# Performance work log

Measured on AMD Instinct MI355X. Metric: run time of the kernel, lower is better.

The kernel has to match this reference:

```python
import jax, jax.numpy as jnp
import numpy as np

B, S, D, H, E, K, F = 2, 2048, 1024, 16, 8, 2, 4096
DH = D // H
EPS = 1e-5


def setup_inputs() -> dict:
    key = jax.random.key(0)
    ks = jax.random.split(key, 10)
    init = lambda k, shape, scale: (jax.random.normal(k, shape, jnp.float32) * scale)
    s_d = D ** -0.5
    s_f = F ** -0.5
    return {
        "x": init(ks[0], (B, S, D), 1.0),
        "attn_mask": jnp.tril(jnp.ones((S, S), bool)),  # causal boolean mask
        "wq": init(ks[1], (D, D), s_d),
        "wk": init(ks[2], (D, D), s_d),
        "wv": init(ks[3], (D, D), s_d),
        "wo": init(ks[4], (D, D), s_d),
        "ln1_g": jnp.ones((D,), jnp.float32),
        "ln1_b": jnp.zeros((D,), jnp.float32),
        "ln2_g": jnp.ones((D,), jnp.float32),
        "ln2_b": jnp.zeros((D,), jnp.float32),
        "gate_w": init(ks[5], (D, E), s_d),
        "e_w1": init(ks[6], (E, D, F), s_d),
        "e_b1": jnp.zeros((E, F), jnp.float32),
        "e_w2": init(ks[7], (E, F, D), s_f),
        "e_b2": jnp.zeros((E, D), jnp.float32),
    }


def _ln(x, g, b):
    m = x.mean(-1, keepdims=True)
    v = ((x - m) ** 2).mean(-1, keepdims=True)
    return (x - m) * jax.lax.rsqrt(v + EPS) * g + b


def _mha(x, attn_mask, wq, wk, wv, wo):
    # x: [B,S,D] -> q,k,v: [B,H,S,DH]
    q = (x @ wq).reshape(B, S, H, DH).transpose(0, 2, 1, 3)
    k = (x @ wk).reshape(B, S, H, DH).transpose(0, 2, 1, 3)
    v = (x @ wv).reshape(B, S, H, DH).transpose(0, 2, 1, 3)
    scores = jnp.einsum("bhqd,bhkd->bhqk", q, k) * (DH ** -0.5)
    scores = jnp.where(attn_mask, scores, jnp.finfo(scores.dtype).min)
    attn = jax.nn.softmax(scores, axis=-1)
    o = jnp.einsum("bhqk,bhkd->bhqd", attn, v)
    return o.transpose(0, 2, 1, 3).reshape(B, S, D) @ wo


def _moe(x, gate_w, e_w1, e_b1, e_w2, e_b2):
    tokens = x.reshape(-1, D)  # [N,D]
    logits = tokens @ gate_w   # [N,E]
    vals, idx = jax.lax.top_k(logits, K)
    tw = jax.nn.softmax(vals, axis=-1)  # softmax over selected top-k logits
    # dense per-token expert weight matrix [N,E] (zero for unselected experts)
    w_dense = (jax.nn.one_hot(idx, E, dtype=tokens.dtype) * tw[..., None]).sum(1)

    def step(acc, p):
        w1, b1, w2, b2, we = p
        h = jax.nn.gelu(tokens @ w1 + b1)
        return acc + (h @ w2 + b2) * we[:, None], None

    combined, _ = jax.lax.scan(
        step, jnp.zeros_like(tokens), (e_w1, e_b1, e_w2, e_b2, w_dense.T)
    )
    return combined.reshape(x.shape)


def reference(x, attn_mask, wq, wk, wv, wo, ln1_g, ln1_b, ln2_g, ln2_b,
              gate_w, e_w1, e_b1, e_w2, e_b2):
    x = _ln(x, ln1_g, ln1_b)
    x = x + _mha(x, attn_mask, wq, wk, wv, wo)  # dropout p=0.0
    x = _ln(x, ln2_g, ln2_b)
    x = x + _moe(x, gate_w, e_w1, e_b1, e_w2, e_b2)
    return x
```

## Files before the change

### kernel.cpp

```cpp
#include <hip/hip_runtime.h>
#include <math.h>
#include <stdint.h>

typedef __attribute__((ext_vector_type(8))) short short8;
typedef __attribute__((ext_vector_type(4))) float f32x4;
typedef __attribute__((ext_vector_type(4))) unsigned short u16x4;

#define NB 2
#define NS 2048
#define ND 1024
#define NH 16
#define NDH 64
#define NE 8
#define NF 4096
#define NTOK 4096
#define MAXBLK 72

__device__ __forceinline__ float bf2f(unsigned short u) {
  union { float f; uint32_t i; } x; x.i = ((uint32_t)u) << 16; return x.f;
}
__device__ __forceinline__ unsigned short f2bf(float f) {
  union { float f; uint32_t i; } x; x.f = f;
  uint32_t r = x.i + 0x7fffu + ((x.i >> 16) & 1u);
  return (unsigned short)(r >> 16);
}
struct bfp { unsigned short h, l; };
__device__ __forceinline__ bfp splitf(float x) {
  bfp r;
  r.h = f2bf(x);
  r.l = f2bf(x - bf2f(r.h));
  return r;
}
__device__ __forceinline__ float gelu_f(float x) {
  float u = 0.7978845608028654f * (x + 0.044715f * x * x * x);
  return 0.5f * x * (1.0f + tanhf(u));
}
#define MFMA(a, b, c) __builtin_amdgcn_mfma_f32_16x16x32_bf16(a, b, c, 0, 0, 0)
__device__ __forceinline__ f32x4 mfma4(short8 ah, short8 al, short8 bh, short8 bl,
                                       f32x4 c) {
  c = MFMA(ah, bh, c);
  c = MFMA(ah, bl, c);
  c = MFMA(al, bh, c);
  c = MFMA(al, bl, c);
  return c;
}

__global__ __launch_bounds__(256) void ln_kernel(
    const float* __restrict__ x, const float* __restrict__ g,
    const float* __restrict__ b, unsigned short* __restrict__ out_h,
    unsigned short* __restrict__ out_l, unsigned short* __restrict__ out_b16,
    float* __restrict__ out_f) {
  int row = blockIdx.x;
  int tid = threadIdx.x;
  const float* xr = x + (size_t)row * ND;
  f32x4 v = *(const f32x4*)(xr + tid * 4);
  float s = v[0] + v[1] + v[2] + v[3];
  float s2 = v[0]*v[0] + v[1]*v[1] + v[2]*v[2] + v[3]*v[3];
  for (int o = 1; o < 64; o <<= 1) { s += __shfl_xor(s, o); s2 += __shfl_xor(s2, o); }
  __shared__ float red[8];
  if ((tid & 63) == 0) { red[tid >> 6] = s; red[4 + (tid >> 6)] = s2; }
  __syncthreads();
  s = red[0] + red[1] + red[2] + red[3];
  s2 = red[4] + red[5] + red[6] + red[7];
  float mean = s * (1.0f / ND);
  float var = s2 * (1.0f / ND) - mean * mean;
  float rstd = rsqrtf(var + 1e-5f);
  f32x4 gg = *(const f32x4*)(g + tid * 4);
  f32x4 bb = *(const f32x4*)(b + tid * 4);
  f32x4 of;
#pragma unroll
  for (int j = 0; j < 4; j++) of[j] = (v[j] - mean) * rstd * gg[j] + bb[j];
  *(f32x4*)(out_f + (size_t)row * ND + tid * 4) = of;
  if (out_h) {
    u16x4 oh, ol;
#pragma unroll
    for (int j = 0; j < 4; j++) { bfp t = splitf(of[j]); oh[j] = t.h; ol[j] = t.l; }
    *(u16x4*)(out_h + (size_t)row * ND + tid * 4) = oh;
    *(u16x4*)(out_l + (size_t)row * ND + tid * 4) = ol;
  }
  if (out_b16) {
    u16x4 ob;
#pragma unroll
    for (int j = 0; j < 4; j++) ob[j] = f2bf(of[j]);
    *(u16x4*)(out_b16 + (size_t)row * ND + tid * 4) = ob;
  }
}

__global__ __launch_bounds__(256) void transpose_wsplit(
    const float* __restrict__ in, unsigned short* __restrict__ outh,
    unsigned short* __restrict__ outl, int R, int C) {
  __shared__ float tile[64][68];
  int r0 = blockIdx.y * 64, c0 = blockIdx.x * 64;
  int lr = threadIdx.x >> 3, lc = (threadIdx.x & 7) * 8;
#pragma unroll
  for (int p = 0; p < 2; p++) {
    int r = lr + p * 32;
    const float* s = in + (size_t)(r0 + r) * C + c0 + lc;
    *(f32x4*)&tile[r][lc] = *(const f32x4*)s;
    *(f32x4*)&tile[r][lc + 4] = *(const f32x4*)(s + 4);
  }
  __syncthreads();
#pragma unroll
  for (int p = 0; p < 2; p++) {
    int c = lr + p * 32;
    u16x4 h0, h1, l0, l1;
#pragma unroll
    for (int i = 0; i < 4; i++) {
      bfp t0 = splitf(tile[lc + i][c]);
      bfp t1 = splitf(tile[lc + 4 + i][c]);
      h0[i] = t0.h; l0[i] = t0.l;
      h1[i] = t1.h; l1[i] = t1.l;
    }
    unsigned short* dh = outh + (size_t)(c0 + c) * R + r0 + lc;
    unsigned short* dl = outl + (size_t)(c0 + c) * R + r0 + lc;
    *(u16x4*)dh = h0; *(u16x4*)(dh + 4) = h1;
    *(u16x4*)dl = l0; *(u16x4*)(dl + 4) = l1;
  }
}

__global__ __launch_bounds__(256) void transpose_w(
    const float* __restrict__ in, unsigned short* __restrict__ out,
    int R, int C) {
  __shared__ unsigned short tile[64][72];
  const float* src = in + (size_t)blockIdx.z * R * C;
  unsigned short* dst = out + (size_t)blockIdx.z * R * C;
  int r0 = blockIdx.y * 64, c0 = blockIdx.x * 64;
  int lr = threadIdx.x >> 3, lc = (threadIdx.x & 7) * 8;
#pragma unroll
  for (int p = 0; p < 2; p++) {
    int r = lr + p * 32;
    const float* s = src + (size_t)(r0 + r) * C + c0 + lc;
    f32x4 a = *(const f32x4*)s;
    f32x4 b = *(const f32x4*)(s + 4);
    u16x4 t0, t1;
#pragma unroll
    for (int j = 0; j < 4; j++) { t0[j] = f2bf(a[j]); t1[j] = f2bf(b[j]); }
    *(u16x4*)&tile[r][lc] = t0;
    *(u16x4*)&tile[r][lc + 4] = t1;
  }
  __syncthreads();
#pragma unroll
  for (int p = 0; p < 2; p++) {
    int c = lr + p * 32;
    union { unsigned short s[8]; f32x4 v; } t;
#pragma unroll
    for (int i = 0; i < 8; i++) t.s[i] = tile[lc + i][c];
    *(f32x4*)(dst + (size_t)(c0 + c) * R + r0 + lc) = t.v;
  }
}

__global__ __launch_bounds__(256) void transpose_v_split(
    const float* __restrict__ v_lin, unsigned short* __restrict__ vth,
    unsigned short* __restrict__ vtl) {
  __shared__ float tile[64][68];
  int bh = blockIdx.y, b = bh >> 4, h = bh & 15;
  int s0 = blockIdx.x * 64;
  int lr = threadIdx.x >> 3, lc = (threadIdx.x & 7) * 8;
#pragma unroll
  for (int p = 0; p < 2; p++) {
    int s = lr + p * 32;
    const float* src = v_lin + (size_t)(b * NS + s0 + s) * ND + h * NDH + lc;
    *(f32x4*)&tile[s][lc] = *(const f32x4*)src;
    *(f32x4*)&tile[s][lc + 4] = *(const f32x4*)(src + 4);
  }
  __syncthreads();
#pragma unroll
  for (int p = 0; p < 2; p++) {
    int dh = lr + p * 32;
    u16x4 h0, h1, l0, l1;
#pragma unroll
    for (int i = 0; i < 4; i++) {
      bfp t0 = splitf(tile[lc + i][dh]);
      bfp t1 = splitf(tile[lc + 4 + i][dh]);
      h0[i] = t0.h; l0[i] = t0.l;
      h1[i] = t1.h; l1[i] = t1.l;
    }
    unsigned short* dh_p = vth + (size_t)(bh * NDH + dh) * NS + s0 + lc;
    unsigned short* dl_p = vtl + (size_t)(bh * NDH + dh) * NS + s0 + lc;
    *(u16x4*)dh_p = h0; *(u16x4*)(dh_p + 4) = h1;
    *(u16x4*)dl_p = l0; *(u16x4*)(dl_p + 4) = l1;
  }
}

template <int MODE>
__global__ __launch_bounds__(256, 2) void gemm_bsplit(
    const unsigned short* __restrict__ Ah, const unsigned short* __restrict__ Al,
    const unsigned short* __restrict__ Bh, const unsigned short* __restrict__ Bl,
    const float* __restrict__ res, float* __restrict__ Cf,
    unsigned short* __restrict__ Ch, unsigned short* __restrict__ Cl,
    int N, int K) {
  __shared__ unsigned short sAh[128 * 72];
  __shared__ unsigned short sAl[128 * 72];
  __shared__ unsigned short sBh[128 * 72];
  __shared__ unsigned short sBl[128 * 72];
  int m0 = blockIdx.y * 128, n0 = blockIdx.x * 128;
  int tid = threadIdx.x;
  int lane = tid & 63, wid = tid >> 6;
  int wy = wid >> 1, wx = wid & 1;
  int col = lane & 15, quad = lane >> 4;
  int srow = tid >> 3, scol = (tid & 7) * 8;
  const unsigned short* ah_p[4];
  const unsigned short* al_p[4];
  const unsigned short* bh_p[4];
  const unsigned short* bl_p[4];
#pragma unroll
  for (int g = 0; g < 4; g++) {
    size_t ao = (size_t)(m0 + g * 32 + srow) * K + scol;
    size_t bo = (size_t)(n0 + g * 32 + srow) * K + scol;
    ah_p[g] = Ah + ao; al_p[g] = Al + ao;
    bh_p[g] = Bh + bo; bl_p[g] = Bl + bo;
  }
  f32x4 acc[4][4];
#pragma unroll
  for (int mt = 0; mt < 4; mt++)
#pragma unroll
    for (int nt = 0; nt < 4; nt++) acc[mt][nt] = (f32x4){0.f, 0.f, 0.f, 0.f};

  for (int k0 = 0; k0 < K; k0 += 64) {
    f32x4 rah[4], ral[4], rbh[4], rbl[4];
#pragma unroll
    for (int g = 0; g < 4; g++) {
      rah[g] = *(const f32x4*)(ah_p[g] + k0);
      ral[g] = *(const f32x4*)(al_p[g] + k0);
      rbh[g] = *(const f32x4*)(bh_p[g] + k0);
      rbl[g] = *(const f32x4*)(bl_p[g] + k0);
    }
    __syncthreads();
#pragma unroll
    for (int g = 0; g < 4; g++) {
      int ro = (g * 32 + srow) * 72 + scol;
      *(f32x4*)(sAh + ro) = rah[g];
      *(f32x4*)(sAl + ro) = ral[g];
      *(f32x4*)(sBh + ro) = rbh[g];
      *(f32x4*)(sBl + ro) = rbl[g];
    }
    __syncthreads();
#pragma unroll
    for (int kk = 0; kk < 2; kk++) {
      short8 ah[4], al[4], bh[4], bl[4];
#pragma unroll
      for (int mt = 0; mt < 4; mt++) {
        int o = (wy * 64 + mt * 16 + col) * 72 + kk * 32 + quad * 8;
        ah[mt] = *(const short8*)(sAh + o);
        al[mt] = *(const short8*)(sAl + o);
      }
#pragma unroll
      for (int nt = 0; nt < 4; nt++) {
        int o = (wx * 64 + nt * 16 + col) * 72 + kk * 32 + quad * 8;
        bh[nt] = *(const short8*)(sBh + o);
        bl[nt] = *(const short8*)(sBl + o);
      }
#pragma unroll
      for (int mt = 0; mt < 4; mt++)
#pragma unroll
        for (int nt = 0; nt < 4; nt++)
          acc[mt][nt] = mfma4(ah[mt], al[mt], bh[nt], bl[nt], acc[mt][nt]);
    }
  }
#pragma unroll
  for (int mt = 0; mt < 4; mt++)
#pragma unroll
    for (int nt = 0; nt < 4; nt++)
#pragma unroll
      for (int r = 0; r < 4; r++) {
        int gr = m0 + wy * 64 + mt * 16 + quad * 4 + r;
        int gc = n0 + wx * 64 + nt * 16 + col;
        float v = acc[mt][nt][r];
        if (MODE == 1) v += res[(size_t)gr * N + gc];
        if (MODE == 2) {
          bfp t = splitf(v);
          Ch[(size_t)gr * N + gc] = t.h;
          Cl[(size_t)gr * N + gc] = t.l;
        } else {
          Cf[(size_t)gr * N + gc] = v;
        }
      }
}

__global__ __launch_bounds__(256, 2) void attn_kernel(
    const unsigned short* __restrict__ qh_g, const unsigned short* __restrict__ ql_g,
    const unsigned short* __restrict__ kh_g, const unsigned short* __restrict__ kl_g,
    const unsigned short* __restrict__ vth_g, const unsigned short* __restrict__ vtl_g,
    unsigned short* __restrict__ oh_g, unsigned short* __restrict__ ol_g) {
  __shared__ unsigned short Kh[64 * 72];
  __shared__ unsigned short Kl[64 * 72];
  __shared__ unsigned short Vh[64 * 72];
  __shared__ unsigned short Vl[64 * 72];
  __shared__ unsigned short Ph[64 * 72];
  __shared__ unsigned short Pl[64 * 72];
  int bh = blockIdx.y, b = bh >> 4, h = bh & 15;
  int tid = threadIdx.x, lane = tid & 63, w = tid >> 6;
  int col = lane & 15, quad = lane >> 4;
  int lr = tid >> 3, lc = (tid & 7) * 8;

  const unsigned short* kbh = kh_g + (size_t)b * NS * ND + h * NDH + lc;
  const unsigned short* kbl = kl_g + (size_t)b * NS * ND + h * NDH + lc;
  const unsigned short* vbh = vth_g + (size_t)bh * NDH * NS;
  const unsigned short* vbl = vtl_g + (size_t)bh * NDH * NS;

#pragma unroll 1
  for (int pass = 0; pass < 2; pass++) {
    int qt = (pass == 0) ? (int)blockIdx.x : 31 - (int)blockIdx.x;
    int q0 = qt * 64;

    size_t qoff = (size_t)(b * NS + q0 + w * 16 + col) * ND + h * NDH;
    short8 qh0 = *(const short8*)(qh_g + qoff + quad * 8);
    short8 qh1 = *(const short8*)(qh_g + qoff + 32 + quad * 8);
    short8 ql0 = *(const short8*)(ql_g + qoff + quad * 8);
    short8 ql1 = *(const short8*)(ql_g + qoff + 32 + quad * 8);

    f32x4 Oa[4];
#pragma unroll
    for (int nt = 0; nt < 4; nt++) Oa[nt] = (f32x4){0.f, 0.f, 0.f, 0.f};
    float mrow[4] = {-1e30f, -1e30f, -1e30f, -1e30f};
    float lrow[4] = {0.f, 0.f, 0.f, 0.f};

    for (int j = 0; j <= qt; j++) {
      __syncthreads();
#pragma unroll
      for (int p = 0; p < 2; p++) {
        int r = lr + p * 32;
        size_t ko = (size_t)(j * 64 + r) * ND;
        size_t vo = (size_t)r * NS + j * 64 + lc;
        *(f32x4*)(Kh + r * 72 + lc) = *(const f32x4*)(kbh + ko);
        *(f32x4*)(Kl + r * 72 + lc) = *(const f32x4*)(kbl + ko);
        *(f32x4*)(Vh + r * 72 + lc) = *(const f32x4*)(vbh + vo);
        *(f32x4*)(Vl + r * 72 + lc) = *(const f32x4*)(vbl + vo);
      }
      __syncthreads();
      f32x4 sf[4];
      __builtin_amdgcn_s_setprio(1);
#pragma unroll
      for (int nt = 0; nt < 4; nt++) {
        int o0 = (nt * 16 + col) * 72 + quad * 8;
        f32x4 a = (f32x4){0.f, 0.f, 0.f, 0.f};
        a = mfma4(qh0, ql0, *(const short8*)(Kh + o0), *(const short8*)(Kl + o0), a);
        a = mfma4(qh1, ql1, *(const short8*)(Kh + o0 + 32), *(const short8*)(Kl + o0 + 32), a);
        sf[nt] = a;
      }
      __builtin_amdgcn_s_setprio(0);
      bool diag = (j == qt);
#pragma unroll
      for (int nt = 0; nt < 4; nt++)
#pragma unroll
        for (int r = 0; r < 4; r++) {
          float v = sf[nt][r] * 0.125f;
          if (diag) {
            int rq = w * 16 + quad * 4 + r;
            int ck = nt * 16 + col;
            if (ck > rq) v = -1e30f;
          }
          sf[nt][r] = v;
        }
#pragma unroll
      for (int r = 0; r < 4; r++) {
        float mx = fmaxf(fmaxf(sf[0][r], sf[1][r]), fmaxf(sf[2][r], sf[3][r]));
        mx = fmaxf(mx, __shfl_xor(mx, 1));
        mx = fmaxf(mx, __shfl_xor(mx, 2));
        mx = fmaxf(mx, __shfl_xor(mx, 4));
        mx = fmaxf(mx, __shfl_xor(mx, 8));
        float mn = fmaxf(mrow[r], mx);
        float al = __expf(mrow[r] - mn);
        mrow[r] = mn;
        float ps = 0.f;
#pragma unroll
        for (int nt = 0; nt < 4; nt++) {
          float p = __expf(sf[nt][r] - mn);
          sf[nt][r] = p;
          ps += p;
        }
        ps += __shfl_xor(ps, 1);
        ps += __shfl_xor(ps, 2);
        ps += __shfl_xor(ps, 4);
        ps += __shfl_xor(ps, 8);
        lrow[r] = lrow[r] * al + ps;
#pragma unroll
        for (int nt = 0; nt < 4; nt++) Oa[nt][r] *= al;
      }
#pragma unroll
      for (int nt = 0; nt < 4; nt++)
#pragma unroll
        for (int r = 0; r < 4; r++) {
          bfp t = splitf(sf[nt][r]);
          int o = (w * 16 + quad * 4 + r) * 72 + nt * 16 + col;
          Ph[o] = t.h;
          Pl[o] = t.l;
        }
      __syncthreads();
      int po = (w * 16 + col) * 72 + quad * 8;
      short8 pf0h = *(const short8*)(Ph + po);
      short8 pf0l = *(const short8*)(Pl + po);
      short8 pf1h = *(const short8*)(Ph + po + 32);
      short8 pf1l = *(const short8*)(Pl + po + 32);
      __builtin_amdgcn_s_setprio(1);
#pragma unroll
      for (int nt = 0; nt < 4; nt++) {
        int o0 = (nt * 16 + col) * 72 + quad * 8;
        Oa[nt] = mfma4(pf0h, pf0l, *(const short8*)(Vh + o0), *(const short8*)(Vl + o0), Oa[nt]);
        Oa[nt] = mfma4(pf1h, pf1l, *(const short8*)(Vh + o0 + 32), *(const short8*)(Vl + o0 + 32), Oa[nt]);
      }
      __builtin_amdgcn_s_setprio(0);
    }
#pragma unroll
    for (int nt = 0; nt < 4; nt++)
#pragma unroll
      for (int r = 0; r < 4; r++) {
        int gr = q0 + w * 16 + quad * 4 + r;
        int gc = nt * 16 + col;
        float ov = Oa[nt][r] / lrow[r];
        bfp t = splitf(ov);
        size_t oo = (size_t)(b * NS + gr) * ND + h * NDH + gc;
        oh_g[oo] = t.h;
        ol_g[oo] = t.l;
      }
  }
}

__device__ __forceinline__ void gemm_mainloop(
    const unsigned short* ap0, const unsigned short* ap1,
    const unsigned short* ap2, const unsigned short* ap3,
    const unsigned short* bp0, const unsigned short* bp1,
    const unsigned short* bp2, const unsigned short* bp3, int K,
    unsigned short* As, unsigned short* Bs, f32x4 acc[4][4]) {
  const int tid = threadIdx.x;
  const int lane = tid & 63, wid = tid >> 6;
  const int wy = wid >> 1, wx = wid & 1;
  const int col = lane & 15, quad = lane >> 4;
  const int srow = tid >> 3, scol = (tid & 7) * 8;
  for (int k0 = 0; k0 < K; k0 += 64) {
    f32x4 ra0 = *(const f32x4*)(ap0 + k0);
    f32x4 ra1 = *(const f32x4*)(ap1 + k0);
    f32x4 ra2 = *(const f32x4*)(ap2 + k0);
    f32x4 ra3 = *(const f32x4*)(ap3 + k0);
    f32x4 rb0 = *(const f32x4*)(bp0 + k0);
    f32x4 rb1 = *(const f32x4*)(bp1 + k0);
    f32x4 rb2 = *(const f32x4*)(bp2 + k0);
    f32x4 rb3 = *(const f32x4*)(bp3 + k0);
    __syncthreads();
    *(f32x4*)(As + (size_t)(srow) * 72 + scol) = ra0;
    *(f32x4*)(As + (size_t)(srow + 32) * 72 + scol) = ra1;
    *(f32x4*)(As + (size_t)(srow + 64) * 72 + scol) = ra2;
    *(f32x4*)(As + (size_t)(srow + 96) * 72 + scol) = ra3;
    *(f32x4*)(Bs + (size_t)(srow) * 72 + scol) = rb0;
    *(f32x4*)(Bs + (size_t)(srow + 32) * 72 + scol) = rb1;
    *(f32x4*)(Bs + (size_t)(srow + 64) * 72 + scol) = rb2;
    *(f32x4*)(Bs + (size_t)(srow + 96) * 72 + scol) = rb3;
    __syncthreads();
#pragma unroll
    for (int kk = 0; kk < 2; kk++) {
      short8 af[4], bfv[4];
#pragma unroll
      for (int mt = 0; mt < 4; mt++)
        af[mt] = *(const short8*)(As + (wy * 64 + mt * 16 + col) * 72 + kk * 32 + quad * 8);
#pragma unroll
      for (int nt = 0; nt < 4; nt++)
        bfv[nt] = *(const short8*)(Bs + (wx * 64 + nt * 16 + col) * 72 + kk * 32 + quad * 8);
#pragma unroll
      for (int mt = 0; mt < 4; mt++)
#pragma unroll
        for (int nt = 0; nt < 4; nt++)
          acc[mt][nt] = MFMA(af[mt], bfv[nt], acc[mt][nt]);
    }
  }
}

__global__ __launch_bounds__(256, 2) void gemm_moe1(
    const unsigned short* __restrict__ x3b, const unsigned short* __restrict__ w1t,
    const float* __restrict__ b1, const int* __restrict__ blk_e,
    const int* __restrict__ blk_mend, const int* __restrict__ tok_list,
    unsigned short* __restrict__ h) {
  __shared__ unsigned short As[128 * 72];
  __shared__ unsigned short Bs[128 * 72];
  int e = blk_e[blockIdx.y];
  if (e < 0) return;
  int mend = blk_mend[blockIdx.y];
  int m0 = blockIdx.y * 128, n0 = blockIdx.x * 128;
  int tid = threadIdx.x;
  int srow = tid >> 3, scol = (tid & 7) * 8;
  const unsigned short* ap[4];
#pragma unroll
  for (int p = 0; p < 4; p++) {
    int gidx = m0 + p * 32 + srow;
    int cl = mend - 1;
    if (gidx < cl) cl = gidx;
    int tok = tok_list[cl];
    ap[p] = x3b + (size_t)tok * ND + scol;
  }
  const unsigned short* bb = w1t + (size_t)e * NF * ND;
  const unsigned short* bp0 = bb + (size_t)(n0 + srow) * ND + scol;
  const unsigned short* bp1 = bb + (size_t)(n0 + 32 + srow) * ND + scol;
  const unsigned short* bp2 = bb + (size_t)(n0 + 64 + srow) * ND + scol;
  const unsigned short* bp3 = bb + (size_t)(n0 + 96 + srow) * ND + scol;
  f32x4 acc[4][4];
#pragma unroll
  for (int mt = 0; mt < 4; mt++)
#pragma unroll
    for (int nt = 0; nt < 4; nt++) acc[mt][nt] = (f32x4){0.f, 0.f, 0.f, 0.f};
  gemm_mainloop(ap[0], ap[1], ap[2], ap[3], bp0, bp1, bp2, bp3, ND, As, Bs, acc);
  int lane = tid & 63, wid = tid >> 6, wy = wid >> 1, wx = wid & 1;
  int col = lane & 15, quad = lane >> 4;
#pragma unroll
  for (int mt = 0; mt < 4; mt++)
#pragma unroll
    for (int nt = 0; nt < 4; nt++)
#pragma unroll
      for (int r = 0; r < 4; r++) {
        int gr = m0 + wy * 64 + mt * 16 + quad * 4 + r;
        if (gr < mend) {
          int gc = n0 + wx * 64 + nt * 16 + col;
          float v = acc[mt][nt][r] + b1[e * NF + gc];
          h[(size_t)gr * NF + gc] = f2bf(gelu_f(v));
        }
      }
}

__global__ __launch_bounds__(256, 2) void gemm_moe2(
    const unsigned short* __restrict__ h, const unsigned short* __restrict__ w2t,
    const float* __restrict__ b2, const int* __restrict__ blk_e,
    const int* __restrict__ blk_mend, const int* __restrict__ tok_list,
    const float* __restrict__ w_list, float* __restrict__ out) {
  __shared__ unsigned short As[128 * 72];
  __shared__ unsigned short Bs[128 * 72];
  int e = blk_e[blockIdx.y];
  if (e < 0) return;
  int mend = blk_mend[blockIdx.y];
  int m0 = blockIdx.y * 128, n0 = blockIdx.x * 128;
  int tid = threadIdx.x;
  int srow = tid >> 3, scol = (tid & 7) * 8;
  const unsigned short* ap0 = h + (size_t)(m0 + srow) * NF + scol;
  const unsigned short* ap1 = h + (size_t)(m0 + 32 + srow) * NF + scol;
  const unsigned short* ap2 = h + (size_t)(m0 + 64 + srow) * NF + scol;
  const unsigned short* ap3 = h + (size_t)(m0 + 96 + srow) * NF + scol;
  const unsigned short* bb = w2t + (size_t)e * ND * NF;
  const unsigned short* bp0 = bb + (size_t)(n0 + srow) * NF + scol;
  const unsigned short* bp1 = bb + (size_t)(n0 + 32 + srow) * NF + scol;
  const unsigned short* bp2 = bb + (size_t)(n0 + 64 + srow) * NF + scol;
  const unsigned short* bp3 = bb + (size_t)(n0 + 96 + srow) * NF + scol;
  f32x4 acc[4][4];
#pragma unroll
  for (int mt = 0; mt < 4; mt++)
#pragma unroll
    for (int nt = 0; nt < 4; nt++) acc[mt][nt] = (f32x4){0.f, 0.f, 0.f, 0.f};
  gemm_mainloop(ap0, ap1, ap2, ap3, bp0, bp1, bp2, bp3, NF, As, Bs, acc);
  int lane = tid & 63, wid = tid >> 6, wy = wid >> 1, wx = wid & 1;
  int col = lane & 15, quad = lane >> 4;
#pragma unroll
  for (int mt = 0; mt < 4; mt++)
#pragma unroll
    for (int nt = 0; nt < 4; nt++)
#pragma unroll
      for (int r = 0; r < 4; r++) {
        int gr = m0 + wy * 64 + mt * 16 + quad * 4 + r;
        if (gr < mend) {
          int gc = n0 + wx * 64 + nt * 16 + col;
          int tok = tok_list[gr];
          float wgt = w_list[gr];
          atomicAdd(&out[(size_t)tok * ND + gc],
                    wgt * (acc[mt][nt][r] + b2[e * ND + gc]));
        }
      }
}

__global__ __launch_bounds__(256) void gate_kernel(
    const float* __restrict__ x3f, const float* __restrict__ gw,
    int* __restrict__ e0a, int* __restrict__ e1a, float* __restrict__ w0a,
    float* __restrict__ w1a, int* __restrict__ cnt) {
  int t = (blockIdx.x * 256 + threadIdx.x) >> 6;
  int lane = threadIdx.x & 63;
  float acc[8] = {0, 0, 0, 0, 0, 0, 0, 0};
  const float* xr = x3f + (size_t)t * ND + lane * 16;
  f32x4 xv[4];
#pragma unroll
  for (int q = 0; q < 4; q++) xv[q] = *(const f32x4*)(xr + q * 4);
#pragma unroll
  for (int i = 0; i < 16; i++) {
    float xval = xv[i >> 2][i & 3];
    const float* grow = gw + (size_t)(lane * 16 + i) * NE;
    f32x4 g0 = *(const f32x4*)grow;
    f32x4 g1 = *(const f32x4*)(grow + 4);
#pragma unroll
    for (int e = 0; e < 4; e++) { acc[e] += xval * g0[e]; acc[4 + e] += xval * g1[e]; }
  }
#pragma unroll
  for (int e = 0; e < 8; e++)
    for (int o = 1; o < 64; o <<= 1) acc[e] += __shfl_xor(acc[e], o);
  if (lane == 0) {
    int i0 = 0;
    float m0 = acc[0];
#pragma unroll
    for (int e = 1; e < 8; e++)
      if (acc[e] > m0) { m0 = acc[e]; i0 = e; }
    int i1 = -1;
    float m1 = -1e30f;
#pragma unroll
    for (int e = 0; e < 8; e++)
      if (e != i0 && acc[e] > m1) { m1 = acc[e]; i1 = e; }
    float sw = __expf(m1 - m0);
    float w0 = 1.f / (1.f + sw);
    e0a[t] = i0; e1a[t] = i1; w0a[t] = w0; w1a[t] = 1.f - w0;
    atomicAdd(&cnt[i0], 1);
    atomicAdd(&cnt[i1], 1);
  }
}

__global__ void moe_scan(const int* __restrict__ cnt, int* __restrict__ seg_off,
                         int* __restrict__ blk_e, int* __restrict__ blk_mend) {
  if (threadIdx.x != 0 || blockIdx.x != 0) return;
  int o = 0, blk = 0;
  for (int e = 0; e < NE; e++) {
    seg_off[e] = o;
    int c = cnt[e];
    int nb = (c + 127) >> 7;
    for (int i = 0; i < nb; i++) { blk_e[blk] = e; blk_mend[blk] = o + c; blk++; }
    o += nb << 7;
  }
  for (; blk < MAXBLK; blk++) blk_e[blk] = -1;
}

__global__ __launch_bounds__(256) void gate_fill(
    const int* __restrict__ e0a, const int* __restrict__ e1a,
    const float* __restrict__ w0a, const float* __restrict__ w1a,
    const int* __restrict__ seg_off, int* __restrict__ fill,
    int* __restrict__ tok_list, float* __restrict__ w_list) {
  int t = blockIdx.x * 256 + threadIdx.x;
  if (t >= NTOK) return;
  int e0 = e0a[t];
  int p0 = seg_off[e0] + atomicAdd(&fill[e0], 1);
  tok_list[p0] = t;
  w_list[p0] = w0a[t];
  int e1 = e1a[t];
  int p1 = seg_off[e1] + atomicAdd(&fill[e1], 1);
  tok_list[p1] = t;
  w_list[p1] = w1a[t];
}

extern "C" void kernel_launch(void* const* d_in, const int* in_sizes, int n_in,
                              void* d_out, int out_size, void* d_ws, size_t ws_size,
                              hipStream_t stream) {
  const float* x = (const float*)d_in[0];
  const float* wq = (const float*)d_in[2];
  const float* wk = (const float*)d_in[3];
  const float* wv = (const float*)d_in[4];
  const float* wo = (const float*)d_in[5];
  const float* ln1g = (const float*)d_in[6];
  const float* ln1b = (const float*)d_in[7];
  const float* ln2g = (const float*)d_in[8];
  const float* ln2b = (const float*)d_in[9];
  const float* gatew = (const float*)d_in[10];
  const float* ew1 = (const float*)d_in[11];
  const float* eb1 = (const float*)d_in[12];
  const float* ew2 = (const float*)d_in[13];
  const float* eb2 = (const float*)d_in[14];
  float* out = (float*)d_out;
  uint8_t* ws = (uint8_t*)d_ws;

  constexpr size_t MB = 1048576;
  constexpr size_t X1F = 0;
  constexpr size_t X1H = 16 * MB;
  constexpr size_t X1L = 24 * MB;
  constexpr size_t QH = 32 * MB;
  constexpr size_t QL = 40 * MB;
  constexpr size_t KH = 48 * MB;
  constexpr size_t KL = 56 * MB;
  constexpr size_t VF = 64 * MB;
  constexpr size_t OH = 64 * MB;
  constexpr size_t OL = 72 * MB;
  constexpr size_t VTH = 80 * MB;
  constexpr size_t VTL = 88 * MB;
  constexpr size_t X2F = 96 * MB;
  constexpr size_t WQTH = 112 * MB;
  constexpr size_t WQTL = 114 * MB;
  constexpr size_t WKTH = 116 * MB;
  constexpr size_t WKTL = 118 * MB;
  constexpr size_t WVTH = 120 * MB;
  constexpr size_t WVTL = 122 * MB;
  constexpr size_t WOTH = 124 * MB;
  constexpr size_t WOTL = 126 * MB;
  constexpr size_t X3B = 128 * MB;
  constexpr size_t HBUF = 136 * MB;
  constexpr size_t W1T = 0;
  constexpr size_t W2T = 64 * MB;
  constexpr size_t CTRL = 208 * MB;
  constexpr size_t CNT = CTRL;
  constexpr size_t FILL = CNT + 32;
  constexpr size_t GE0 = CNT + 64;
  constexpr size_t GE1 = GE0 + 16384;
  constexpr size_t GW0 = GE1 + 16384;
  constexpr size_t GW1 = GW0 + 16384;
  constexpr size_t SEGO = GW1 + 16384;
  constexpr size_t BLKE = SEGO + 64;
  constexpr size_t BLKM = BLKE + 512;
  constexpr size_t TOKL = BLKM + 512;
  constexpr size_t WLST = TOKL + 36864;

  float* pX1F = (float*)(ws + X1F);
  unsigned short* pX1H = (unsigned short*)(ws + X1H);
  unsigned short* pX1L = (unsigned short*)(ws + X1L);
  unsigned short* pQH = (unsigned short*)(ws + QH);
  unsigned short* pQL = (unsigned short*)(ws + QL);
  unsigned short* pKH = (unsigned short*)(ws + KH);
  unsigned short* pKL = (unsigned short*)(ws + KL);
  float* pVF = (float*)(ws + VF);
  unsigned short* pOH = (unsigned short*)(ws + OH);
  unsigned short* pOL = (unsigned short*)(ws + OL);
  unsigned short* pVTH = (unsigned short*)(ws + VTH);
  unsigned short* pVTL = (unsigned short*)(ws + VTL);
  float* pX2F = (float*)(ws + X2F);
  unsigned short* pWQTH = (unsigned short*)(ws + WQTH);
  unsigned short* pWQTL = (unsigned short*)(ws + WQTL);
  unsigned short* pWKTH = (unsigned short*)(ws + WKTH);
  unsigned short* pWKTL = (unsigned short*)(ws + WKTL);
  unsigned short* pWVTH = (unsigned short*)(ws + WVTH);
  unsigned short* pWVTL = (unsigned short*)(ws + WVTL);
  unsigned short* pWOTH = (unsigned short*)(ws + WOTH);
  unsigned short* pWOTL = (unsigned short*)(ws + WOTL);
  unsigned short* pX3B = (unsigned short*)(ws + X3B);
  unsigned short* pH = (unsigned short*)(ws + HBUF);
  unsigned short* pW1T = (unsigned short*)(ws + W1T);
  unsigned short* pW2T = (unsigned short*)(ws + W2T);
  int* pCNT = (int*)(ws + CNT);
  int* pFILL = (int*)(ws + FILL);
  int* pGE0 = (int*)(ws + GE0);
  int* pGE1 = (int*)(ws + GE1);
  float* pGW0 = (float*)(ws + GW0);
  float* pGW1 = (float*)(ws + GW1);
  int* pSEGO = (int*)(ws + SEGO);
  int* pBLKE = (int*)(ws + BLKE);
  int* pBLKM = (int*)(ws + BLKM);
  int* pTOKL = (int*)(ws + TOKL);
  float* pWLST = (float*)(ws + WLST);

  (void)hipMemsetAsync(ws + CNT, 0, 64, stream);

  ln_kernel<<<NTOK, 256, 0, stream>>>(x, ln1g, ln1b, pX1H, pX1L, nullptr, pX1F);

  transpose_wsplit<<<dim3(16, 16), 256, 0, stream>>>(wq, pWQTH, pWQTL, 1024, 1024);
  transpose_wsplit<<<dim3(16, 16), 256, 0, stream>>>(wk, pWKTH, pWKTL, 1024, 1024);
  transpose_wsplit<<<dim3(16, 16), 256, 0, stream>>>(wv, pWVTH, pWVTL, 1024, 1024);
  transpose_wsplit<<<dim3(16, 16), 256, 0, stream>>>(wo, pWOTH, pWOTL, 1024, 1024);

  gemm_bsplit<2><<<dim3(8, 32), 256, 0, stream>>>(
      pX1H, pX1L, pWQTH, pWQTL, nullptr, nullptr, pQH, pQL, ND, ND);
  gemm_bsplit<2><<<dim3(8, 32), 256, 0, stream>>>(
      pX1H, pX1L, pWKTH, pWKTL, nullptr, nullptr, pKH, pKL, ND, ND);
  gemm_bsplit<0><<<dim3(8, 32), 256, 0, stream>>>(
      pX1H, pX1L, pWVTH, pWVTL, nullptr, pVF, nullptr, nullptr, ND, ND);

  transpose_v_split<<<dim3(32, 32), 256, 0, stream>>>(pVF, pVTH, pVTL);
  attn_kernel<<<dim3(16, 32), 256, 0, stream>>>(pQH, pQL, pKH, pKL, pVTH, pVTL, pOH, pOL);
  gemm_bsplit<1><<<dim3(8, 32), 256, 0, stream>>>(
      pOH, pOL, pWOTH, pWOTL, pX1F, pX2F, nullptr, nullptr, ND, ND);

  ln_kernel<<<NTOK, 256, 0, stream>>>(pX2F, ln2g, ln2b, nullptr, nullptr, pX3B, out);

  transpose_w<<<dim3(64, 16, 8), 256, 0, stream>>>(ew1, pW1T, 1024, 4096);
  transpose_w<<<dim3(16, 64, 8), 256, 0, stream>>>(ew2, pW2T, 4096, 1024);

  gate_kernel<<<1024, 256, 0, stream>>>(out, gatew, pGE0, pGE1, pGW0, pGW1, pCNT);
  moe_scan<<<1, 1, 0, stream>>>(pCNT, pSEGO, pBLKE, pBLKM);
  gate_fill<<<16, 256, 0, stream>>>(pGE0, pGE1, pGW0, pGW1, pSEGO, pFILL, pTOKL, pWLST);

  gemm_moe1<<<dim3(32, MAXBLK), 256, 0, stream>>>(pX3B, pW1T, eb1, pBLKE, pBLKM, pTOKL, pH);
  gemm_moe2<<<dim3(8, MAXBLK), 256, 0, stream>>>(pH, pW2T, eb2, pBLKE, pBLKM, pTOKL, pWLST, out);
}
```

Baseline: 1.055 ms.

## Use direct global-to-LDS loads in GEMMs and merge QKV projections into one launch

Replaces the register-staged global loads and LDS stores in all GEMM mainloops with global_load_lds direct copies into a k-chunk-major shared layout. The per-thread load pointer is now a single row per lane, and MFMA operand reads index the new layout. The three Q/K/V projection launches are merged into one gemm_qkv grid with a z dimension selecting the weight and output. This is meant to cut VGPR pressure and load/store instructions and to save two launches. In exchange, the padded layout is dropped, so LDS bank conflicts may increase.

```diff
diff --git a/kernel.cpp b/kernel.cpp
--- a/kernel.cpp
+++ b/kernel.cpp
@@ -43,6 +43,12 @@
   c = MFMA(al, bh, c);
   c = MFMA(al, bl, c);
   return c;
+}
+
+__device__ __forceinline__ void gld16(const unsigned short* g, unsigned short* l) {
+  __builtin_amdgcn_global_load_lds(
+      (__attribute__((address_space(1))) void*)(const void*)g,
+      (__attribute__((address_space(3))) void*)l, 16, 0, 0);
 }
 
 __global__ __launch_bounds__(256) void ln_kernel(
@@ -182,81 +188,129 @@
   }
 }
 
-template <int MODE>
-__global__ __launch_bounds__(256, 2) void gemm_bsplit(
-    const unsigned short* __restrict__ Ah, const unsigned short* __restrict__ Al,
-    const unsigned short* __restrict__ Bh, const unsigned short* __restrict__ Bl,
-    const float* __restrict__ res, float* __restrict__ Cf,
-    unsigned short* __restrict__ Ch, unsigned short* __restrict__ Cl,
-    int N, int K) {
-  __shared__ unsigned short sAh[128 * 72];
-  __shared__ unsigned short sAl[128 * 72];
-  __shared__ unsigned short sBh[128 * 72];
-  __shared__ unsigned short sBl[128 * 72];
+
+__device__ __forceinline__ void bsplit_mainloop(
+    const unsigned short* ahr, const unsigned short* alr,
+    const unsigned short* bhr, const unsigned short* blr, int K,
+    unsigned short* sAh, unsigned short* sAl,
+    unsigned short* sBh, unsigned short* sBl, f32x4 acc[4][4]) {
+  const int tid = threadIdx.x;
+  const int lane = tid & 63, wid = tid >> 6;
+  const int wy = wid >> 1, wx = wid & 1;
+  const int col = lane & 15, quad = lane >> 4;
+  const int rg = wid >> 1, c0 = (wid & 1) * 4;
+  (void)lane;
+  for (int k0 = 0; k0 < K; k0 += 64) {
+    __syncthreads();
+#pragma unroll
+    for (int j = 0; j < 4; j++) {
+      int c = c0 + j;
+      int d = c * 1024 + rg * 512;
+      int s = k0 + c * 8;
+      gld16(ahr + s, sAh + d);
+      gld16(alr + s, sAl + d);
+      gld16(bhr + s, sBh + d);
+      gld16(blr + s, sBl + d);
+    }
+    __syncthreads();
+#pragma unroll
+    for (int kk = 0; kk < 2; kk++) {
+      short8 ah[4], al[4], bh[4], bl[4];
+#pragma unroll
+      for (int mt = 0; mt < 4; mt++) {
+        int o = (kk * 4 + quad) * 1024 + (wy * 64 + mt * 16 + col) * 8;
+        ah[mt] = *(const short8*)(sAh + o);
+        al[mt] = *(const short8*)(sAl + o);
+      }
+#pragma unroll
+      for (int nt = 0; nt < 4; nt++) {
+        int o = (kk * 4 + quad) * 1024 + (wx * 64 + nt * 16 + col) * 8;
+        bh[nt] = *(const short8*)(sBh + o);
+        bl[nt] = *(const short8*)(sBl + o);
+      }
+#pragma unroll
+      for (int mt = 0; mt < 4; mt++)
+#pragma unroll
+        for (int nt = 0; nt < 4; nt++)
+          acc[mt][nt] = mfma4(ah[mt], al[mt], bh[nt], bl[nt], acc[mt][nt]);
+    }
+  }
+}
+
+__device__ __forceinline__ void moe_mainloop(
+    const unsigned short* ar, const unsigned short* br, int K,
+    unsigned short* As, unsigned short* Bs, f32x4 acc[4][4]) {
+  const int tid = threadIdx.x;
+  const int lane = tid & 63, wid = tid >> 6;
+  const int wy = wid >> 1, wx = wid & 1;
+  const int col = lane & 15, quad = lane >> 4;
+  const int rg = wid >> 1, c0 = (wid & 1) * 4;
+  (void)lane;
+  for (int k0 = 0; k0 < K; k0 += 64) {
+    __syncthreads();
+#pragma unroll
+    for (int j = 0; j < 4; j++) {
+      int c = c0 + j;
+      int d = c * 1024 + rg * 512;
+      int s = k0 + c * 8;
+      gld16(ar + s, As + d);
+      gld16(br + s, Bs + d);
+    }
+    __syncthreads();
+#pragma unroll
+    for (int kk = 0; kk < 2; kk++) {
+      short8 af[4], bfv[4];
+#pragma unroll
+      for (int mt = 0; mt < 4; mt++)
+        af[mt] = *(const short8*)(As + (kk * 4 + quad) * 1024 + (wy * 64 + mt * 16 + col) * 8);
+#pragma unroll
+      for (int nt = 0; nt < 4; nt++)
+        bfv[nt] = *(const short8*)(Bs + (kk * 4 + quad) * 1024 + (wx * 64 + nt * 16 + col) * 8);
+#pragma unroll
+      for (int mt = 0; mt < 4; mt++)
+#pragma unroll
+        for (int nt = 0; nt < 4; nt++)
+          acc[mt][nt] = MFMA(af[mt], bfv[nt], acc[mt][nt]);
+    }
+  }
+}
+
+__global__ __launch_bounds__(256, 2) void gemm_qkv(
+    const unsigned short* __restrict__ Xh, const unsigned short* __restrict__ Xl,
+    const unsigned short* __restrict__ wqh, const unsigned short* __restrict__ wql,
+    const unsigned short* __restrict__ wkh, const unsigned short* __restrict__ wkl,
+    const unsigned short* __restrict__ wvh, const unsigned short* __restrict__ wvl,
+    unsigned short* __restrict__ qh, unsigned short* __restrict__ ql,
+    unsigned short* __restrict__ kh, unsigned short* __restrict__ kl,
+    float* __restrict__ vf) {
+  __shared__ __attribute__((aligned(16))) unsigned short sAh[8192];
+  __shared__ __attribute__((aligned(16))) unsigned short sAl[8192];
+  __shared__ __attribute__((aligned(16))) unsigned short sBh[8192];
+  __shared__ __attribute__((aligned(16))) unsigned short sBl[8192];
+  int z = blockIdx.z;
+  const unsigned short* Bh = (z == 0) ? wqh : (z == 1) ? wkh : wvh;
+  const unsigned short* Bl = (z == 0) ? wql : (z == 1) ? wkl : wvl;
+  unsigned short* oh = (z == 0) ? qh : kl ? kh : kh;
+  unsigned short* ol;
+  if (z == 0) { oh = qh; ol = ql; } else { oh = kh; ol = kl; }
   int m0 = blockIdx.y * 128, n0 = blockIdx.x * 128;
   int tid = threadIdx.x;
   int lane = tid & 63, wid = tid >> 6;
+  int rg = wid >> 1;
+  int row_a = m0 + rg * 64 + lane;
+  int row_b = n0 + rg * 64 + lane;
+  const unsigned short* ahr = Xh + (size_t)row_a * ND;
+  const unsigned short* alr = Xl + (size_t)row_a * ND;
+  const unsigned short* bhr = Bh + (size_t)row_b * ND;
+  const unsigned short* blr = Bl + (size_t)row_b * ND;
+  f32x4 acc[4][4];
+#pragma unroll
+  for (int mt = 0; mt < 4; mt++)
+#pragma unroll
+    for (int nt = 0; nt < 4; nt++) acc[mt][nt] = (f32x4){0.f, 0.f, 0.f, 0.f};
+  bsplit_mainloop(ahr, alr, bhr, blr, ND, sAh, sAl, sBh, sBl, acc);
   int wy = wid >> 1, wx = wid & 1;
   int col = lane & 15, quad = lane >> 4;
-  int srow = tid >> 3, scol = (tid & 7) * 8;
-  const unsigned short* ah_p[4];
-  const unsigned short* al_p[4];
-  const unsigned short* bh_p[4];
-  const unsigned short* bl_p[4];
-#pragma unroll
-  for (int g = 0; g < 4; g++) {
-    size_t ao = (size_t)(m0 + g * 32 + srow) * K + scol;
-    size_t bo = (size_t)(n0 + g * 32 + srow) * K + scol;
-    ah_p[g] = Ah + ao; al_p[g] = Al + ao;
-    bh_p[g] = Bh + bo; bl_p[g] = Bl + bo;
-  }
-  f32x4 acc[4][4];
-#pragma unroll
-  for (int mt = 0; mt < 4; mt++)
-#pragma unroll
-    for (int nt = 0; nt < 4; nt++) acc[mt][nt] = (f32x4){0.f, 0.f, 0.f, 0.f};
-
-  for (int k0 = 0; k0 < K; k0 += 64) {
-    f32x4 rah[4], ral[4], rbh[4], rbl[4];
-#pragma unroll
-    for (int g = 0; g < 4; g++) {
-      rah[g] = *(const f32x4*)(ah_p[g] + k0);
-      ral[g] = *(const f32x4*)(al_p[g] + k0);
-      rbh[g] = *(const f32x4*)(bh_p[g] + k0);
-      rbl[g] = *(const f32x4*)(bl_p[g] + k0);
-    }
-    __syncthreads();
-#pragma unroll
-    for (int g = 0; g < 4; g++) {
-      int ro = (g * 32 + srow) * 72 + scol;
-      *(f32x4*)(sAh + ro) = rah[g];
-      *(f32x4*)(sAl + ro) = ral[g];
-      *(f32x4*)(sBh + ro) = rbh[g];
-      *(f32x4*)(sBl + ro) = rbl[g];
-    }
-    __syncthreads();
-#pragma unroll
-    for (int kk = 0; kk < 2; kk++) {
-      short8 ah[4], al[4], bh[4], bl[4];
-#pragma unroll
-      for (int mt = 0; mt < 4; mt++) {
-        int o = (wy * 64 + mt * 16 + col) * 72 + kk * 32 + quad * 8;
-        ah[mt] = *(const short8*)(sAh + o);
-        al[mt] = *(const short8*)(sAl + o);
-      }
-#pragma unroll
-      for (int nt = 0; nt < 4; nt++) {
-        int o = (wx * 64 + nt * 16 + col) * 72 + kk * 32 + quad * 8;
-        bh[nt] = *(const short8*)(sBh + o);
-        bl[nt] = *(const short8*)(sBl + o);
-      }
-#pragma unroll
-      for (int mt = 0; mt < 4; mt++)
-#pragma unroll
-        for (int nt = 0; nt < 4; nt++)
-          acc[mt][nt] = mfma4(ah[mt], al[mt], bh[nt], bl[nt], acc[mt][nt]);
-    }
-  }
 #pragma unroll
   for (int mt = 0; mt < 4; mt++)
 #pragma unroll
@@ -266,14 +320,49 @@
         int gr = m0 + wy * 64 + mt * 16 + quad * 4 + r;
         int gc = n0 + wx * 64 + nt * 16 + col;
         float v = acc[mt][nt][r];
-        if (MODE == 1) v += res[(size_t)gr * N + gc];
-        if (MODE == 2) {
+        if (z == 2) {
+          vf[(size_t)gr * ND + gc] = v;
+        } else {
           bfp t = splitf(v);
-          Ch[(size_t)gr * N + gc] = t.h;
-          Cl[(size_t)gr * N + gc] = t.l;
-        } else {
-          Cf[(size_t)gr * N + gc] = v;
+          oh[(size_t)gr * ND + gc] = t.h;
+          ol[(size_t)gr * ND + gc] = t.l;
         }
+      }
+}
+
+__global__ __launch_bounds__(256, 2) void gemm_oproj(
+    const unsigned short* __restrict__ Ah, const unsigned short* __restrict__ Al,
+    const unsigned short* __restrict__ Bh, const unsigned short* __restrict__ Bl,
+    const float* __restrict__ res, float* __restrict__ Cf) {
+  __shared__ __attribute__((aligned(16))) unsigned short sAh[8192];
+  __shared__ __attribute__((aligned(16))) unsigned short sAl[8192];
+  __shared__ __attribute__((aligned(16))) unsigned short sBh[8192];
+  __shared__ __attribute__((aligned(16))) unsigned short sBl[8192];
+  int m0 = blockIdx.y * 128, n0 = blockIdx.x * 128;
+  int tid = threadIdx.x;
+  int lane = tid & 63, wid = tid >> 6;
+  int rg = wid >> 1;
+  const unsigned short* ahr = Ah + (size_t)(m0 + rg * 64 + lane) * ND;
+  const unsigned short* alr = Al + (size_t)(m0 + rg * 64 + lane) * ND;
+  const unsigned short* bhr = Bh + (size_t)(n0 + rg * 64 + lane) * ND;
+  const unsigned short* blr = Bl + (size_t)(n0 + rg * 64 + lane) * ND;
+  f32x4 acc[4][4];
+#pragma unroll
+  for (int mt = 0; mt < 4; mt++)
+#pragma unroll
+    for (int nt = 0; nt < 4; nt++) acc[mt][nt] = (f32x4){0.f, 0.f, 0.f, 0.f};
+  bsplit_mainloop(ahr, alr, bhr, blr, ND, sAh, sAl, sBh, sBl, acc);
+  int wy = wid >> 1, wx = wid & 1;
+  int col = lane & 15, quad = lane >> 4;
+#pragma unroll
+  for (int mt = 0; mt < 4; mt++)
+#pragma unroll
+    for (int nt = 0; nt < 4; nt++)
+#pragma unroll
+      for (int r = 0; r < 4; r++) {
+        int gr = m0 + wy * 64 + mt * 16 + quad * 4 + r;
+        int gc = n0 + wx * 64 + nt * 16 + col;
+        Cf[(size_t)gr * ND + gc] = acc[mt][nt][r] + res[(size_t)gr * ND + gc];
       }
 }
 
@@ -416,88 +505,32 @@
   }
 }
 
-__device__ __forceinline__ void gemm_mainloop(
-    const unsigned short* ap0, const unsigned short* ap1,
-    const unsigned short* ap2, const unsigned short* ap3,
-    const unsigned short* bp0, const unsigned short* bp1,
-    const unsigned short* bp2, const unsigned short* bp3, int K,
-    unsigned short* As, unsigned short* Bs, f32x4 acc[4][4]) {
-  const int tid = threadIdx.x;
-  const int lane = tid & 63, wid = tid >> 6;
-  const int wy = wid >> 1, wx = wid & 1;
-  const int col = lane & 15, quad = lane >> 4;
-  const int srow = tid >> 3, scol = (tid & 7) * 8;
-  for (int k0 = 0; k0 < K; k0 += 64) {
-    f32x4 ra0 = *(const f32x4*)(ap0 + k0);
-    f32x4 ra1 = *(const f32x4*)(ap1 + k0);
-    f32x4 ra2 = *(const f32x4*)(ap2 + k0);
-    f32x4 ra3 = *(const f32x4*)(ap3 + k0);
-    f32x4 rb0 = *(const f32x4*)(bp0 + k0);
-    f32x4 rb1 = *(const f32x4*)(bp1 + k0);
-    f32x4 rb2 = *(const f32x4*)(bp2 + k0);
-    f32x4 rb3 = *(const f32x4*)(bp3 + k0);
-    __syncthreads();
-    *(f32x4*)(As + (size_t)(srow) * 72 + scol) = ra0;
-    *(f32x4*)(As + (size_t)(srow + 32) * 72 + scol) = ra1;
-    *(f32x4*)(As + (size_t)(srow + 64) * 72 + scol) = ra2;
-    *(f32x4*)(As + (size_t)(srow + 96) * 72 + scol) = ra3;
-    *(f32x4*)(Bs + (size_t)(srow) * 72 + scol) = rb0;
-    *(f32x4*)(Bs + (size_t)(srow + 32) * 72 + scol) = rb1;
-    *(f32x4*)(Bs + (size_t)(srow + 64) * 72 + scol) = rb2;
-    *(f32x4*)(Bs + (size_t)(srow + 96) * 72 + scol) = rb3;
-    __syncthreads();
-#pragma unroll
-    for (int kk = 0; kk < 2; kk++) {
-      short8 af[4], bfv[4];
-#pragma unroll
-      for (int mt = 0; mt < 4; mt++)
-        af[mt] = *(const short8*)(As + (wy * 64 + mt * 16 + col) * 72 + kk * 32 + quad * 8);
-#pragma unroll
-      for (int nt = 0; nt < 4; nt++)
-        bfv[nt] = *(const short8*)(Bs + (wx * 64 + nt * 16 + col) * 72 + kk * 32 + quad * 8);
-#pragma unroll
-      for (int mt = 0; mt < 4; mt++)
-#pragma unroll
-        for (int nt = 0; nt < 4; nt++)
-          acc[mt][nt] = MFMA(af[mt], bfv[nt], acc[mt][nt]);
-    }
-  }
-}
-
 __global__ __launch_bounds__(256, 2) void gemm_moe1(
     const unsigned short* __restrict__ x3b, const unsigned short* __restrict__ w1t,
     const float* __restrict__ b1, const int* __restrict__ blk_e,
     const int* __restrict__ blk_mend, const int* __restrict__ tok_list,
     unsigned short* __restrict__ h) {
-  __shared__ unsigned short As[128 * 72];
-  __shared__ unsigned short Bs[128 * 72];
+  __shared__ __attribute__((aligned(16))) unsigned short As[8192];
+  __shared__ __attribute__((aligned(16))) unsigned short Bs[8192];
   int e = blk_e[blockIdx.y];
   if (e < 0) return;
   int mend = blk_mend[blockIdx.y];
   int m0 = blockIdx.y * 128, n0 = blockIdx.x * 128;
   int tid = threadIdx.x;
-  int srow = tid >> 3, scol = (tid & 7) * 8;
-  const unsigned short* ap[4];
-#pragma unroll
-  for (int p = 0; p < 4; p++) {
-    int gidx = m0 + p * 32 + srow;
-    int cl = mend - 1;
-    if (gidx < cl) cl = gidx;
-    int tok = tok_list[cl];
-    ap[p] = x3b + (size_t)tok * ND + scol;
-  }
-  const unsigned short* bb = w1t + (size_t)e * NF * ND;
-  const unsigned short* bp0 = bb + (size_t)(n0 + srow) * ND + scol;
-  const unsigned short* bp1 = bb + (size_t)(n0 + 32 + srow) * ND + scol;
-  const unsigned short* bp2 = bb + (size_t)(n0 + 64 + srow) * ND + scol;
-  const unsigned short* bp3 = bb + (size_t)(n0 + 96 + srow) * ND + scol;
+  int lane = tid & 63, wid = tid >> 6;
+  int rg = wid >> 1;
+  int gidx = m0 + rg * 64 + lane;
+  int cl = gidx < (mend - 1) ? gidx : (mend - 1);
+  int tok = tok_list[cl];
+  const unsigned short* ar = x3b + (size_t)tok * ND;
+  const unsigned short* br = w1t + (size_t)e * NF * ND + (size_t)(n0 + rg * 64 + lane) * ND;
   f32x4 acc[4][4];
 #pragma unroll
   for (int mt = 0; mt < 4; mt++)
 #pragma unroll
     for (int nt = 0; nt < 4; nt++) acc[mt][nt] = (f32x4){0.f, 0.f, 0.f, 0.f};
-  gemm_mainloop(ap[0], ap[1], ap[2], ap[3], bp0, bp1, bp2, bp3, ND, As, Bs, acc);
-  int lane = tid & 63, wid = tid >> 6, wy = wid >> 1, wx = wid & 1;
+  moe_mainloop(ar, br, ND, As, Bs, acc);
+  int wy = wid >> 1, wx = wid & 1;
   int col = lane & 15, quad = lane >> 4;
 #pragma unroll
   for (int mt = 0; mt < 4; mt++)
@@ -519,30 +552,24 @@
     const float* __restrict__ b2, const int* __restrict__ blk_e,
     const int* __restrict__ blk_mend, const int* __restrict__ tok_list,
     const float* __restrict__ w_list, float* __restrict__ out) {
-  __shared__ unsigned short As[128 * 72];
-  __shared__ unsigned short Bs[128 * 72];
+  __shared__ __attribute__((aligned(16))) unsigned short As[8192];
+  __shared__ __attribute__((aligned(16))) unsigned short Bs[8192];
   int e = blk_e[blockIdx.y];
   if (e < 0) return;
   int mend = blk_mend[blockIdx.y];
   int m0 = blockIdx.y * 128, n0 = blockIdx.x * 128;
   int tid = threadIdx.x;
-  int srow = tid >> 3, scol = (tid & 7) * 8;
-  const unsigned short* ap0 = h + (size_t)(m0 + srow) * NF + scol;
-  const unsigned short* ap1 = h + (size_t)(m0 + 32 + srow) * NF + scol;
-  const unsigned short* ap2 = h + (size_t)(m0 + 64 + srow) * NF + scol;
-  const unsigned short* ap3 = h + (size_t)(m0 + 96 + srow) * NF + scol;
-  const unsigned short* bb = w2t + (size_t)e * ND * NF;
-  const unsigned short* bp0 = bb + (size_t)(n0 + srow) * NF + scol;
-  const unsigned short* bp1 = bb + (size_t)(n0 + 32 + srow) * NF + scol;
-  const unsigned short* bp2 = bb + (size_t)(n0 + 64 + srow) * NF + scol;
-  const unsigned short* bp3 = bb + (size_t)(n0 + 96 + srow) * NF + scol;
+  int lane = tid & 63, wid = tid >> 6;
+  int rg = wid >> 1;
+  const unsigned short* ar = h + (size_t)(m0 + rg * 64 + lane) * NF;
+  const unsigned short* br = w2t + (size_t)e * ND * NF + (size_t)(n0 + rg * 64 + lane) * NF;
   f32x4 acc[4][4];
 #pragma unroll
   for (int mt = 0; mt < 4; mt++)
 #pragma unroll
     for (int nt = 0; nt < 4; nt++) acc[mt][nt] = (f32x4){0.f, 0.f, 0.f, 0.f};
-  gemm_mainloop(ap0, ap1, ap2, ap3, bp0, bp1, bp2, bp3, NF, As, Bs, acc);
-  int lane = tid & 63, wid = tid >> 6, wy = wid >> 1, wx = wid & 1;
+  moe_mainloop(ar, br, NF, As, Bs, acc);
+  int wy = wid >> 1, wx = wid & 1;
   int col = lane & 15, quad = lane >> 4;
 #pragma unroll
   for (int mt = 0; mt < 4; mt++)
@@ -739,17 +766,13 @@
   transpose_wsplit<<<dim3(16, 16), 256, 0, stream>>>(wv, pWVTH, pWVTL, 1024, 1024);
   transpose_wsplit<<<dim3(16, 16), 256, 0, stream>>>(wo, pWOTH, pWOTL, 1024, 1024);
 
-  gemm_bsplit<2><<<dim3(8, 32), 256, 0, stream>>>(
-      pX1H, pX1L, pWQTH, pWQTL, nullptr, nullptr, pQH, pQL, ND, ND);
-  gemm_bsplit<2><<<dim3(8, 32), 256, 0, stream>>>(
-      pX1H, pX1L, pWKTH, pWKTL, nullptr, nullptr, pKH, pKL, ND, ND);
-  gemm_bsplit<0><<<dim3(8, 32), 256, 0, stream>>>(
-      pX1H, pX1L, pWVTH, pWVTL, nullptr, pVF, nullptr, nullptr, ND, ND);
+  gemm_qkv<<<dim3(8, 32, 3), 256, 0, stream>>>(
+      pX1H, pX1L, pWQTH, pWQTL, pWKTH, pWKTL, pWVTH, pWVTL,
+      pQH, pQL, pKH, pKL, pVF);
 
   transpose_v_split<<<dim3(32, 32), 256, 0, stream>>>(pVF, pVTH, pVTL);
   attn_kernel<<<dim3(16, 32), 256, 0, stream>>>(pQH, pQL, pKH, pKL, pVTH, pVTL, pOH, pOL);
-  gemm_bsplit<1><<<dim3(8, 32), 256, 0, stream>>>(
-      pOH, pOL, pWOTH, pWOTL, pX1F, pX2F, nullptr, nullptr, ND, ND);
+  gemm_oproj<<<dim3(8, 32), 256, 0, stream>>>(pOH, pOL, pWOTH, pWOTL, pX1F, pX2F);
 
   ln_kernel<<<NTOK, 256, 0, stream>>>(pX2F, ln2g, ln2b, nullptr, nullptr, pX3B, out);
 
```

Measured after the change: 1.310 ms. 24.2% more time.
